# Performance work log

Measured on AMD Instinct MI355X. Metric: run time of the kernel, lower is better.

The kernel has to match this reference:

```python
import jax, jax.numpy as jnp
import numpy as np

HORIZON = 2048
TAU = 0.06


def setup_inputs() -> dict:
    key = jax.random.key(0)
    k1, k2, k3 = jax.random.split(key, 3)
    B = 4096
    d = jax.random.normal(k1, (B, HORIZON, 1), dtype=jnp.float32)
    W1 = jax.random.normal(k2, (2, 64), dtype=jnp.float32) * 0.5
    b1 = jnp.zeros((64,), dtype=jnp.float32)
    W2 = jax.random.normal(k3, (64, 2), dtype=jnp.float32) * 0.5
    b2 = jnp.zeros((2,), dtype=jnp.float32)
    return {"d": d, "W1": W1, "b1": b1, "W2": W2, "b2": b2}


def _controller(x, dt, W1, b1, W2, b2):
    # x, dt: [B, 1] -> u, u_bin: [B, 1]
    h = jnp.tanh(jnp.concatenate([x, dt], axis=-1) @ W1 + b1)
    z = h @ W2 + b2
    u = z[:, 0:1]
    u_bin = jax.nn.sigmoid(z[:, 1:2] / TAU)  # soft binary control (hard=False)
    return u, u_bin


def reference(d, W1, b1, W2, b2):
    B = d.shape[0]
    x0 = d[:, 0, :]                      # [B, 1] initial state = d[:, 0:1, :]
    heating0 = jnp.ones_like(x0)         # thermostat relay state, init 1

    def step(carry, dt):
        x, heating = carry
        u, u_bin = _controller(x, dt, W1, b1, W2, b2)
        on = x < 8.0
        off = x > 12.0
        heating = jnp.where(on, 1.0, jnp.where(off, 0.0, heating))
        u_applied = u_bin * 0.4          # neural=True branch: binary * 0.4
        x_new = 0.99 * x + u_applied - dt
        return (x_new, heating), (x_new, u)

    # steps t = 1 .. horizon-2  -> horizon-2 steps
    d_seq = jnp.transpose(d[:, 1:HORIZON - 1, :], (1, 0, 2))  # [T, B, 1]
    (_, _), (xs_t, us_t) = jax.lax.scan(step, (x0, heating0), d_seq)

    xs = jnp.concatenate([x0[:, None, :], jnp.transpose(xs_t, (1, 0, 2))], axis=1)
    us = jnp.concatenate([jnp.zeros((B, 1, 1), dtype=d.dtype), jnp.transpose(us_t, (1, 0, 2))], axis=1)
    return xs, us
```

## Files before the change

### kernel.cpp

```cpp
#include <hip/hip_runtime.h>

#define HORIZON 2048
#define B_TOTAL 4096
#define T_OUT 2047

__device__ __forceinline__ float hw_exp2(float x) {
    float r;
    asm("v_exp_f32 %0, %1" : "=v"(r) : "v"(x));
    return r;
}
__device__ __forceinline__ float hw_rcp(float x) {
    float r;
    asm("v_rcp_f32 %0, %1" : "=v"(r) : "v"(x));
    return r;
}

template<int CTRL>
__device__ __forceinline__ float dpp_mov(float v) {
    return __int_as_float(__builtin_amdgcn_update_dpp(
        0, __float_as_int(v), CTRL, 0xF, 0xF, true));
}

__device__ __forceinline__ float rowsum16(float v) {
    v += dpp_mov<0xB1>(v);
    v += dpp_mov<0x4E>(v);
    v += dpp_mov<0x124>(v);
    v += dpp_mov<0x128>(v);
    return v;
}

#define K1  2.8853900817779268f
#define CS -24.04491734814939f

__global__ __launch_bounds__(64) void thermostat_scan4(
    const float* __restrict__ d,
    const float* __restrict__ W1,
    const float* __restrict__ b1,
    const float* __restrict__ W2,
    const float* __restrict__ b2,
    float* __restrict__ xs,
    float* __restrict__ us)
{
    const int lane = threadIdx.x;
    const int sub  = lane >> 4;
    const int pos  = lane & 15;
    const int grow = blockIdx.x * 4 + sub;

    const float* drow = d + (size_t)grow * HORIZON;
    const float4* dv  = (const float4*)drow;

    float w10c[4], w11c[4], b1c[4], w20m[4], w21m[4];
    float s20p = 0.f, s21p = 0.f;
#pragma unroll
    for (int k = 0; k < 4; ++k) {
        int j = pos + 16 * k;
        w10c[k] = W1[j] * K1;
        w11c[k] = W1[64 + j] * K1;
        b1c[k]  = b1[j] * K1;
        float a0 = W2[2 * j], a1 = W2[2 * j + 1];
        w20m[k] = -2.f * a0;
        w21m[k] = -2.f * a1;
        s20p += a0;
        s21p += a1;
    }
    const float zb0  = rowsum16(s20p) + b2[0];
    const float zb1c = (rowsum16(s21p) + b2[1]) * CS;

    float* xs_p = xs + (size_t)grow * T_OUT + pos;
    float* us_p = us + (size_t)grow * T_OUT + pos;

    float4 c0 = dv[0], c1 = dv[1], c2 = dv[2], c3 = dv[3];
    float4 n0 = dv[4], n1 = dv[5], n2 = dv[6], n3 = dv[7];

    float x = c0.x;
    float keep_x = x;
    float keep_u = -zb0;

    auto step = [&](float dt, int slot) {
        float e0 = hw_exp2(fmaf(x, w10c[0], fmaf(dt, w11c[0], b1c[0])));
        float e1 = hw_exp2(fmaf(x, w10c[1], fmaf(dt, w11c[1], b1c[1])));
        float e2 = hw_exp2(fmaf(x, w10c[2], fmaf(dt, w11c[2], b1c[2])));
        float e3 = hw_exp2(fmaf(x, w10c[3], fmaf(dt, w11c[3], b1c[3])));
        float r0 = hw_rcp(e0 + 1.f);
        float r1 = hw_rcp(e1 + 1.f);
        float r2 = hw_rcp(e2 + 1.f);
        float r3 = hw_rcp(e3 + 1.f);
        float q1a = fmaf(r1, w21m[1], r0 * w21m[0]);
        float q1b = fmaf(r3, w21m[3], r2 * w21m[2]);
        float z1  = rowsum16(q1a + q1b);
        float q0a = fmaf(r1, w20m[1], r0 * w20m[0]);
        float q0b = fmaf(r3, w20m[3], r2 * w20m[2]);
        float z0  = rowsum16(q0a + q0b);
        float ub = hw_rcp(1.f + hw_exp2(fmaf(z1, CS, zb1c)));
        x = fmaf(0.99f, x, fmaf(0.4f, ub, -dt));
        bool k = (pos == slot);
        keep_x = k ? x : keep_x;
        keep_u = k ? z0 : keep_u;
    };

    {
        float dt16[16] = {c0.x, c0.y, c0.z, c0.w, c1.x, c1.y, c1.z, c1.w,
                          c2.x, c2.y, c2.z, c2.w, c3.x, c3.y, c3.z, c3.w};
#pragma unroll
        for (int s = 1; s < 16; ++s) step(dt16[s], s);
        xs_p[0] = keep_x;
        us_p[0] = keep_u + zb0;
    }

    for (int c = 1; c < 127; ++c) {
        c0 = n0; c1 = n1; c2 = n2; c3 = n3;
        n0 = dv[4 * c + 4]; n1 = dv[4 * c + 5];
        n2 = dv[4 * c + 6]; n3 = dv[4 * c + 7];
        float dt16[16] = {c0.x, c0.y, c0.z, c0.w, c1.x, c1.y, c1.z, c1.w,
                          c2.x, c2.y, c2.z, c2.w, c3.x, c3.y, c3.z, c3.w};
#pragma unroll
        for (int s = 0; s < 16; ++s) step(dt16[s], s);
        xs_p[c * 16] = keep_x;
        us_p[c * 16] = keep_u + zb0;
    }

    {
        float dt16[16] = {n0.x, n0.y, n0.z, n0.w, n1.x, n1.y, n1.z, n1.w,
                          n2.x, n2.y, n2.z, n2.w, n3.x, n3.y, n3.z, n3.w};
#pragma unroll
        for (int s = 0; s < 15; ++s) step(dt16[s], s);
        if (pos < 15) {
            xs_p[127 * 16] = keep_x;
            us_p[127 * 16] = keep_u + zb0;
        }
    }
}

extern "C" void kernel_launch(void* const* d_in, const int* in_sizes, int n_in,
                              void* d_out, int out_size, void* d_ws, size_t ws_size,
                              hipStream_t stream) {
    const float* d  = (const float*)d_in[0];
    const float* W1 = (const float*)d_in[1];
    const float* b1 = (const float*)d_in[2];
    const float* W2 = (const float*)d_in[3];
    const float* b2 = (const float*)d_in[4];
    float* xs = (float*)d_out;
    float* us = xs + (size_t)B_TOTAL * T_OUT;

    dim3 grid(B_TOTAL / 4);
    thermostat_scan4<<<grid, 64, 0, stream>>>(d, W1, b1, W2, b2, xs, us);
}
```

Baseline: 222.4 us.

## Pack hidden-layer math into float2, share reciprocals, precompute next-step dt terms

```diff
diff --git a/kernel.cpp b/kernel.cpp
--- a/kernel.cpp
+++ b/kernel.cpp
@@ -3,6 +3,8 @@
 #define HORIZON 2048
 #define B_TOTAL 4096
 #define T_OUT 2047
+
+typedef float v2f __attribute__((ext_vector_type(2)));
 
 __device__ __forceinline__ float hw_exp2(float x) {
     float r;
@@ -31,6 +33,7 @@
 
 #define K1  2.8853900817779268f
 #define CS -24.04491734814939f
+#define ACLAMP 60.0f
 
 __global__ __launch_bounds__(64) void thermostat_scan4(
     const float* __restrict__ d,
@@ -49,19 +52,22 @@
     const float* drow = d + (size_t)grow * HORIZON;
     const float4* dv  = (const float4*)drow;
 
-    float w10c[4], w11c[4], b1c[4], w20m[4], w21m[4];
+    v2f w10c[2], w11c[2], b1c[2];
+    float w20m[4], w21m[4];
     float s20p = 0.f, s21p = 0.f;
 #pragma unroll
-    for (int k = 0; k < 4; ++k) {
-        int j = pos + 16 * k;
-        w10c[k] = W1[j] * K1;
-        w11c[k] = W1[64 + j] * K1;
-        b1c[k]  = b1[j] * K1;
-        float a0 = W2[2 * j], a1 = W2[2 * j + 1];
-        w20m[k] = -2.f * a0;
-        w21m[k] = -2.f * a1;
-        s20p += a0;
-        s21p += a1;
+    for (int p = 0; p < 2; ++p) {
+        int j0 = pos + 16 * (2 * p);
+        int j1 = pos + 16 * (2 * p + 1);
+        w10c[p] = v2f{W1[j0] * K1, W1[j1] * K1};
+        w11c[p] = v2f{W1[64 + j0] * K1, W1[64 + j1] * K1};
+        b1c[p]  = v2f{b1[j0] * K1, b1[j1] * K1};
+        float a00 = W2[2 * j0], a01 = W2[2 * j0 + 1];
+        float a10 = W2[2 * j1], a11 = W2[2 * j1 + 1];
+        w20m[2 * p]     = -2.f * a00;  w21m[2 * p]     = -2.f * a01;
+        w20m[2 * p + 1] = -2.f * a10;  w21m[2 * p + 1] = -2.f * a11;
+        s20p += a00 + a10;
+        s21p += a01 + a11;
     }
     const float zb0  = rowsum16(s20p) + b2[0];
     const float zb1c = (rowsum16(s21p) + b2[1]) * CS;
@@ -76,23 +82,40 @@
     float keep_x = x;
     float keep_u = -zb0;
 
-    auto step = [&](float dt, int slot) {
-        float e0 = hw_exp2(fmaf(x, w10c[0], fmaf(dt, w11c[0], b1c[0])));
-        float e1 = hw_exp2(fmaf(x, w10c[1], fmaf(dt, w11c[1], b1c[1])));
-        float e2 = hw_exp2(fmaf(x, w10c[2], fmaf(dt, w11c[2], b1c[2])));
-        float e3 = hw_exp2(fmaf(x, w10c[3], fmaf(dt, w11c[3], b1c[3])));
-        float r0 = hw_rcp(e0 + 1.f);
-        float r1 = hw_rcp(e1 + 1.f);
-        float r2 = hw_rcp(e2 + 1.f);
-        float r3 = hw_rcp(e3 + 1.f);
-        float q1a = fmaf(r1, w21m[1], r0 * w21m[0]);
-        float q1b = fmaf(r3, w21m[3], r2 * w21m[2]);
-        float z1  = rowsum16(q1a + q1b);
-        float q0a = fmaf(r1, w20m[1], r0 * w20m[0]);
-        float q0b = fmaf(r3, w20m[3], r2 * w20m[2]);
-        float z0  = rowsum16(q0a + q0b);
+    v2f db0, db1;
+    {
+        v2f dt2 = v2f{c0.y, c0.y};
+        db0 = dt2 * w11c[0] + b1c[0];
+        db1 = dt2 * w11c[1] + b1c[1];
+    }
+
+    const v2f clo = v2f{-ACLAMP, -ACLAMP};
+    const v2f chi = v2f{ ACLAMP,  ACLAMP};
+
+    auto step = [&](float dt, float dtn, int slot) {
+        v2f x2 = v2f{x, x};
+        v2f a0 = x2 * w10c[0] + db0;
+        v2f a1 = x2 * w10c[1] + db1;
+        a0 = __builtin_elementwise_min(__builtin_elementwise_max(a0, clo), chi);
+        a1 = __builtin_elementwise_min(__builtin_elementwise_max(a1, clo), chi);
+        v2f s0 = v2f{hw_exp2(a0.x), hw_exp2(a0.y)} + v2f{1.f, 1.f};
+        v2f s1 = v2f{hw_exp2(a1.x), hw_exp2(a1.y)} + v2f{1.f, 1.f};
+        float rp0 = hw_rcp(s0.x * s0.y);
+        float rp1 = hw_rcp(s1.x * s1.y);
+        float r0 = s0.y * rp0, r1 = s0.x * rp0;
+        float r2 = s1.y * rp1, r3 = s1.x * rp1;
+        float q1 = fmaf(r1, w21m[1], r0 * w21m[0])
+                 + fmaf(r3, w21m[3], r2 * w21m[2]);
+        float z1 = rowsum16(q1);
+        float q0 = fmaf(r1, w20m[1], r0 * w20m[0])
+                 + fmaf(r3, w20m[3], r2 * w20m[2]);
+        float z0 = rowsum16(q0);
+        float xd = fmaf(0.99f, x, -dt);
+        v2f dtn2 = v2f{dtn, dtn};
+        db0 = dtn2 * w11c[0] + b1c[0];
+        db1 = dtn2 * w11c[1] + b1c[1];
         float ub = hw_rcp(1.f + hw_exp2(fmaf(z1, CS, zb1c)));
-        x = fmaf(0.99f, x, fmaf(0.4f, ub, -dt));
+        x = fmaf(0.4f, ub, xd);
         bool k = (pos == slot);
         keep_x = k ? x : keep_x;
         keep_u = k ? z0 : keep_u;
@@ -102,7 +125,8 @@
         float dt16[16] = {c0.x, c0.y, c0.z, c0.w, c1.x, c1.y, c1.z, c1.w,
                           c2.x, c2.y, c2.z, c2.w, c3.x, c3.y, c3.z, c3.w};
 #pragma unroll
-        for (int s = 1; s < 16; ++s) step(dt16[s], s);
+        for (int s = 1; s < 16; ++s)
+            step(dt16[s], (s < 15) ? dt16[s + 1] : n0.x, s);
         xs_p[0] = keep_x;
         us_p[0] = keep_u + zb0;
     }
@@ -114,7 +138,8 @@
         float dt16[16] = {c0.x, c0.y, c0.z, c0.w, c1.x, c1.y, c1.z, c1.w,
                           c2.x, c2.y, c2.z, c2.w, c3.x, c3.y, c3.z, c3.w};
 #pragma unroll
-        for (int s = 0; s < 16; ++s) step(dt16[s], s);
+        for (int s = 0; s < 16; ++s)
+            step(dt16[s], (s < 15) ? dt16[s + 1] : n0.x, s);
         xs_p[c * 16] = keep_x;
         us_p[c * 16] = keep_u + zb0;
     }
@@ -123,7 +148,8 @@
         float dt16[16] = {n0.x, n0.y, n0.z, n0.w, n1.x, n1.y, n1.z, n1.w,
                           n2.x, n2.y, n2.z, n2.w, n3.x, n3.y, n3.z, n3.w};
 #pragma unroll
-        for (int s = 0; s < 15; ++s) step(dt16[s], s);
+        for (int s = 0; s < 15; ++s)
+            step(dt16[s], dt16[s + 1], s);
         if (pos < 15) {
             xs_p[127 * 16] = keep_x;
             us_p[127 * 16] = keep_u + zb0;
```

Result: slower. 251.2 us (+13.0%).
